# Kernel optimization log

Hardware: AMD Instinct MI355X
Metric: run time of the kernel (lower is better)

The kernel has to match this reference:

```python
import jax, jax.numpy as jnp
import numpy as np

B, T, C, H, E, L = 4, 1024, 768, 12, 4, 2
DH = C // H


def setup_inputs() -> dict:
    key = jax.random.key(0)
    ks = jax.random.split(key, 10)
    s = 0.02  # init scale; keeps unscaled-attention logits sane (source has no 1/sqrt(d))
    w = lambda k, shape: (jax.random.normal(k, shape, jnp.float32) * s)
    z = lambda shape: jnp.zeros(shape, jnp.float32)
    return dict(
        x=jax.random.normal(ks[0], (B, T, C), jnp.float32),
        gate_W=w(ks[1], (C, E)), gate_b=z((E,)),
        Wq=w(ks[2], (E, L, C, C)), bq=z((E, L, C)),
        Wk=w(ks[3], (E, L, C, C)), bk=z((E, L, C)),
        Wv=w(ks[4], (E, L, C, C)), bv=z((E, L, C)),
        Wo=w(ks[5], (E, L, C, C)), bo=z((E, L, C)),
        ln_g=jnp.ones((E, L, C), jnp.float32), ln_b=z((E, L, C)),
        Wfc=w(ks[6], (E, L, C, 4 * C)), bfc=z((E, L, 4 * C)),
        Wpr=w(ks[7], (E, L, 4 * C, C)), bpr=z((E, L, C)),
    )


def _attn(x, Wq, bq, Wk, bk, Wv, bv, Wo, bo):
    # FlashAttention3 blockwise loop == exact full softmax(Q K^T) V, NO scaling, NO mask
    q = (x @ Wq + bq).reshape(B, T, H, DH)
    k = (x @ Wk + bk).reshape(B, T, H, DH)
    v = (x @ Wv + bv).reshape(B, T, H, DH)
    s = jnp.einsum('bqhd,bkhd->bhqk', q, k)
    p = jax.nn.softmax(s, axis=-1)
    o = jnp.einsum('bhqk,bkhd->bqhd', p, v).reshape(B, T, C)
    return o @ Wo + bo


def _ln(x, g, b, eps=1e-5):
    m = x.mean(-1, keepdims=True)
    v = ((x - m) ** 2).mean(-1, keepdims=True)
    return (x - m) * jax.lax.rsqrt(v + eps) * g + b


def _expert(x, Wq, bq, Wk, bk, Wv, bv, Wo, bo, ln_g, ln_b, Wfc, bfc, Wpr, bpr):
    # Sequential(attn, layernorm, mlp) x L — no residuals, dropout=0 (eval)
    for l in range(L):
        x = _attn(x, Wq[l], bq[l], Wk[l], bk[l], Wv[l], bv[l], Wo[l], bo[l])
        x = _ln(x, ln_g[l], ln_b[l])
        h = jax.nn.gelu(x @ Wfc[l] + bfc[l], approximate=True)  # tanh GELU
        x = h @ Wpr[l] + bpr[l]
    return x


def reference(x, gate_W, gate_b, Wq, bq, Wk, bk, Wv, bv, Wo, bo,
              ln_g, ln_b, Wfc, bfc, Wpr, bpr):
    gate_probs = jax.nn.softmax(x @ gate_W + gate_b, axis=-1)  # [B,T,E]
    expert_fn = jax.vmap(_expert, in_axes=(None,) + (0,) * 14)
    eo = expert_fn(x, Wq, bq, Wk, bk, Wv, bv, Wo, bo, ln_g, ln_b, Wfc, bfc, Wpr, bpr)  # [E,B,T,C]
    return jnp.einsum('bte,ebtc->btc', gate_probs, eo)
```

## Files before the change

### kernel.cpp

```cpp
#include <hip/hip_runtime.h>

#define B_ 4
#define T_ 1024
#define C_ 768
#define H_ 12
#define E_ 4
#define L_ 2
#define DH_ 64
#define M_ (B_*T_)
#define QKVS_ (3*C_)
#define LOG2E_ 1.4426950408889634f

typedef __attribute__((ext_vector_type(8))) short bf16x8;
typedef __attribute__((ext_vector_type(4))) float f32x4;

__device__ __forceinline__ unsigned short f2bf(float f) {
  unsigned int u = __float_as_uint(f);
  unsigned int r = (u + 0x7FFFu + ((u >> 16) & 1u)) >> 16;
  return (unsigned short)r;
}
__device__ __forceinline__ float bf2f(unsigned short s) {
  return __uint_as_float(((unsigned int)s) << 16);
}
__device__ __forceinline__ unsigned int cvt_pk_bf16(float lo, float hi) {
  unsigned int r;
  asm("v_cvt_pk_bf16_f32 %0, %1, %2" : "=v"(r) : "v"(lo), "v"(hi));
  return r;
}

typedef __attribute__((address_space(1))) unsigned int gu32;
typedef __attribute__((address_space(3))) unsigned int lu32;
__device__ __forceinline__ void gld_lds16(const void* g, void* l) {
  __builtin_amdgcn_global_load_lds((gu32*)g, (lu32*)l, 16, 0, 0);
}

__device__ __forceinline__ float gelu_fast(float x) {
  float u = 0.7978845608028654f * x * (1.0f + 0.044715f * x * x);
  float d = 1.0f + exp2f(-2.8853900817779268f * u);
  return x * __builtin_amdgcn_rcpf(d);
}

template <int ACT>
__global__ __launch_bounds__(512, 2) void gemm256(
    const unsigned short* __restrict__ A, const unsigned short* __restrict__ Bt,
    const float* __restrict__ bias, unsigned short* __restrict__ D,
    int M, int N, int K, long long sA, long long sB, long long sBias, long long sD,
    float bscale)
{
  __shared__ unsigned short shA[2][256*64];
  __shared__ unsigned short shB[2][256*64];
  const int tid = threadIdx.x;
  const int lane = tid & 63, wid = tid >> 6;
  const int l15 = lane & 15, lhi = lane >> 4;
  const int wm = wid >> 2, wn = wid & 3;
  const int m0 = blockIdx.y * 256, n0 = blockIdx.x * 256;
  const int g = blockIdx.z;
  const unsigned short* Ab = A + (size_t)g * sA;
  const unsigned short* Bb = Bt + (size_t)g * sB;
  const float* biasb = bias + (size_t)g * sBias;
  unsigned short* Db = D + (size_t)g * sD;

  f32x4 acc[8][4] = {};

  const int srow = tid >> 3;
  const int schk = (((tid & 7) ^ (srow & 7)) << 3);
  auto stage = [&](int buf, int k0) {
    #pragma unroll
    for (int p = 0; p < 4; ++p)
      gld_lds16(Ab + (size_t)(m0 + p*64 + srow) * K + (k0 + schk), &shA[buf][p*4096 + tid*8]);
    #pragma unroll
    for (int p = 0; p < 4; ++p)
      gld_lds16(Bb + (size_t)(n0 + p*64 + srow) * K + (k0 + schk), &shB[buf][p*4096 + tid*8]);
  };

  const int swz = l15 & 7;
  const int ca0 = (lhi ^ swz) << 3;
  const int ca1 = ((4 + lhi) ^ swz) << 3;

  auto compute = [&](int buf) {
    #pragma unroll
    for (int kh = 0; kh < 2; ++kh) {
      const int cc = kh ? ca1 : ca0;
      bf16x8 bfrag[4];
      #pragma unroll
      for (int nf = 0; nf < 4; ++nf)
        bfrag[nf] = *(const bf16x8*)&shB[buf][(wn*64 + nf*16 + l15)*64 + cc];
      #pragma unroll
      for (int mh = 0; mh < 2; ++mh) {
        bf16x8 afr[4];
        #pragma unroll
        for (int i = 0; i < 4; ++i)
          afr[i] = *(const bf16x8*)&shA[buf][(wm*128 + (mh*4 + i)*16 + l15)*64 + cc];
        __builtin_amdgcn_s_setprio(1);
        #pragma unroll
        for (int i = 0; i < 4; ++i)
          #pragma unroll
          for (int nf = 0; nf < 4; ++nf)
            acc[mh*4+i][nf] = __builtin_amdgcn_mfma_f32_16x16x32_bf16(
                afr[i], bfrag[nf], acc[mh*4+i][nf], 0, 0, 0);
        __builtin_amdgcn_s_setprio(0);
      }
    }
  };

  const int nkt = K >> 6;
  stage(0, 0);
  stage(1, 64);

  for (int kt = 0; kt < nkt - 2; ++kt) {
    asm volatile("s_waitcnt vmcnt(8)" ::: "memory");
    __builtin_amdgcn_s_barrier();
    compute(kt & 1);
    __builtin_amdgcn_s_barrier();
    stage(kt & 1, (kt + 2) << 6);
  }
  asm volatile("s_waitcnt vmcnt(8)" ::: "memory");
  __builtin_amdgcn_s_barrier();
  compute((nkt - 2) & 1);
  asm volatile("s_waitcnt vmcnt(0)" ::: "memory");
  __builtin_amdgcn_s_barrier();
  compute((nkt - 1) & 1);

  #pragma unroll
  for (int nf = 0; nf < 4; ++nf) {
    const int col = n0 + wn*64 + nf*16 + l15;
    const float bv = bscale * biasb[col];
    #pragma unroll
    for (int mf = 0; mf < 8; ++mf) {
      const int r0 = m0 + wm*128 + mf*16 + lhi*4;
      #pragma unroll
      for (int r = 0; r < 4; ++r) {
        float v = acc[mf][nf][r] + bv;
        if (ACT == 1) v = gelu_fast(v);
        Db[(size_t)(r0 + r) * N + col] = f2bf(v);
      }
    }
  }
}

__global__ __launch_bounds__(256) void flash_attn(
    const unsigned short* __restrict__ qkv, const unsigned short* __restrict__ vt,
    unsigned short* __restrict__ o)
{
  __shared__ unsigned short shK[2][64*64];
  __shared__ unsigned short shV[2][64*64];
  __shared__ unsigned short shP[4][16*64];
  const int tid = threadIdx.x;
  const int wid = tid >> 6, lane = tid & 63;
  const int l15 = lane & 15, lhi = lane >> 4;
  const int qt = blockIdx.x, h = blockIdx.y, eb = blockIdx.z;

  const unsigned short* qrow = qkv + ((size_t)eb*T_ + qt*64 + wid*16 + l15) * QKVS_ + h*DH_;
  bf16x8 aq0 = *(const bf16x8*)(qrow + lhi*8);
  bf16x8 aq1 = *(const bf16x8*)(qrow + 32 + lhi*8);

  f32x4 oacc[4] = {};
  float lpart = 0.f;

  const int krow = tid >> 3;
  const int swzsrc = (((tid & 7) ^ (krow & 7)) << 3);
  const unsigned short* kbase = qkv + (size_t)eb*T_*QKVS_ + C_ + h*DH_;
  const unsigned short* vbase = vt + ((size_t)eb*H_ + h)*DH_*T_;

  auto stage = [&](int buf, int kt) {
    #pragma unroll
    for (int p = 0; p < 2; ++p) {
      gld_lds16(kbase + (size_t)(kt*64 + krow + p*32)*QKVS_ + swzsrc,
                &shK[buf][(p*256 + wid*64)*8]);
      gld_lds16(vbase + (size_t)(krow + p*32)*T_ + kt*64 + swzsrc,
                &shV[buf][(p*256 + wid*64)*8]);
    }
  };

  stage(0, 0);
  __syncthreads();
  int cur = 0;
  const int swzr = l15 & 7;
  const int c0 = (lhi ^ swzr) << 3;
  const int c1 = ((4 + lhi) ^ swzr) << 3;
  const int pwbase = l15*64 + ((lhi & 1) << 2);
  const int pwh = lhi >> 1;

  for (int kt = 0; kt < T_/64; ++kt) {
    if (kt + 1 < T_/64) stage(cur ^ 1, kt + 1);

    f32x4 s[4];
    #pragma unroll
    for (int kb = 0; kb < 4; ++kb) {
      const int row = (kb*16 + l15)*64;
      bf16x8 bk0 = *(const bf16x8*)&shK[cur][row + c0];
      bf16x8 bk1 = *(const bf16x8*)&shK[cur][row + c1];
      f32x4 z = {};
      z = __builtin_amdgcn_mfma_f32_16x16x32_bf16(bk0, aq0, z, 0, 0, 0);
      s[kb] = __builtin_amdgcn_mfma_f32_16x16x32_bf16(bk1, aq1, z, 0, 0, 0);
    }
    unsigned int pk0[4], pk1[4];
    #pragma unroll
    for (int kb = 0; kb < 4; ++kb) {
      #pragma unroll
      for (int r = 0; r < 4; ++r) {
        float pv = exp2f(s[kb][r]);
        s[kb][r] = pv;
        lpart += pv;
      }
      pk0[kb] = cvt_pk_bf16(s[kb][0], s[kb][1]);
      pk1[kb] = cvt_pk_bf16(s[kb][2], s[kb][3]);
    }
    #pragma unroll
    for (int kb = 0; kb < 4; ++kb) {
      const int chunk = (2*kb + pwh) ^ swzr;
      uint2 w = {pk0[kb], pk1[kb]};
      *(uint2*)&shP[wid][pwbase + chunk*8] = w;
    }
    bf16x8 pa0 = *(const bf16x8*)&shP[wid][l15*64 + c0];
    bf16x8 pa1 = *(const bf16x8*)&shP[wid][l15*64 + c1];
    #pragma unroll
    for (int n = 0; n < 4; ++n) {
      const int row = (n*16 + l15)*64;
      bf16x8 bv0 = *(const bf16x8*)&shV[cur][row + c0];
      bf16x8 bv1 = *(const bf16x8*)&shV[cur][row + c1];
      oacc[n] = __builtin_amdgcn_mfma_f32_16x16x32_bf16(pa0, bv0, oacc[n], 0, 0, 0);
      oacc[n] = __builtin_amdgcn_mfma_f32_16x16x32_bf16(pa1, bv1, oacc[n], 0, 0, 0);
    }
    __syncthreads();
    cur ^= 1;
  }
  lpart += __shfl_xor(lpart, 16);
  lpart += __shfl_xor(lpart, 32);
  float li[4];
  #pragma unroll
  for (int r = 0; r < 4; ++r) li[r] = __shfl(lpart, lhi*4 + r);
  #pragma unroll
  for (int n = 0; n < 4; ++n)
    #pragma unroll
    for (int r = 0; r < 4; ++r) {
      float v = oacc[n][r] / li[r];
      o[((size_t)eb*T_ + qt*64 + wid*16 + lhi*4 + r) * C_ + h*DH_ + n*16 + l15] = f2bf(v);
    }
}

__global__ void transpose_cast(const float* __restrict__ in, unsigned short* __restrict__ out,
                               int K, int N, long long inStride, long long outStride, float scale)
{
  __shared__ float tile[32][33];
  const float* src = in + (size_t)blockIdx.z * inStride;
  unsigned short* dst = out + (size_t)blockIdx.z * outStride;
  const int tx = threadIdx.x, ty = threadIdx.y;
  const int k0 = blockIdx.y*32, n0 = blockIdx.x*32;
  #pragma unroll
  for (int j = 0; j < 32; j += 8)
    tile[ty+j][tx] = src[(size_t)(k0+ty+j)*N + n0+tx];
  __syncthreads();
  #pragma unroll
  for (int j = 0; j < 32; j += 8)
    dst[(size_t)(n0+ty+j)*K + k0+tx] = f2bf(scale * tile[tx][ty+j]);
}

__global__ __launch_bounds__(256) void build_qkv_bias(
    const float* __restrict__ bq, const float* __restrict__ bk, const float* __restrict__ bv,
    float* __restrict__ dst, int l)
{
  const int i = blockIdx.x*256 + threadIdx.x;
  const int g = i / C_, c = i - g*C_;
  const size_t src = ((size_t)g*L_ + l)*C_ + c;
  dst[(size_t)g*QKVS_ + c]        = LOG2E_ * bq[src];
  dst[(size_t)g*QKVS_ + C_ + c]   = bk[src];
  dst[(size_t)g*QKVS_ + 2*C_ + c] = bv[src];
}

__global__ void transpose_v_kernel(const unsigned short* __restrict__ qkv, unsigned short* __restrict__ vt)
{
  __shared__ unsigned short tile[32][33];
  const int t0 = blockIdx.x * 32, d0 = blockIdx.y * 32;
  const int z = blockIdx.z;
  const int h = z % H_, eb = z / H_;
  const int tx = threadIdx.x, ty = threadIdx.y;
  #pragma unroll
  for (int j = 0; j < 32; j += 8)
    tile[ty+j][tx] = qkv[((size_t)eb*T_ + t0+ty+j)*QKVS_ + 2*C_ + h*DH_ + d0 + tx];
  __syncthreads();
  #pragma unroll
  for (int j = 0; j < 32; j += 8)
    vt[((size_t)z*DH_ + d0+ty+j)*T_ + t0 + tx] = tile[tx][ty+j];
}

__global__ __launch_bounds__(256) void ln_kernel(
    const unsigned short* __restrict__ in, unsigned short* __restrict__ out,
    const float* __restrict__ g, const float* __restrict__ b)
{
  const int row = blockIdx.x * 4 + (threadIdx.x >> 6);
  const int lane = threadIdx.x & 63;
  const int e = row >> 12;
  const unsigned short* ir = in + (size_t)row * C_;
  unsigned short* orow = out + (size_t)row * C_;
  const float* gg = g + (size_t)e * (L_*C_);
  const float* bb = b + (size_t)e * (L_*C_);
  float v[12]; float s = 0.f, s2 = 0.f;
  #pragma unroll
  for (int j = 0; j < 12; ++j) {
    float x = bf2f(ir[lane + 64*j]);
    v[j] = x; s += x; s2 += x*x;
  }
  #pragma unroll
  for (int d = 32; d; d >>= 1) { s += __shfl_xor(s, d); s2 += __shfl_xor(s2, d); }
  float mean = s * (1.f/C_);
  float var = s2 * (1.f/C_) - mean*mean;
  float rstd = rsqrtf(var + 1e-5f);
  #pragma unroll
  for (int j = 0; j < 12; ++j) {
    int c = lane + 64*j;
    orow[c] = f2bf((v[j]-mean)*rstd*gg[c] + bb[c]);
  }
}

__global__ __launch_bounds__(256) void gate_kernel(
    const float* __restrict__ x, const float* __restrict__ gw, const float* __restrict__ gb,
    float* __restrict__ gp)
{
  const int row = blockIdx.x * 4 + (threadIdx.x >> 6);
  const int lane = threadIdx.x & 63;
  const float* xr = x + (size_t)row * C_;
  float a0=0.f, a1=0.f, a2=0.f, a3=0.f;
  for (int i = lane; i < C_; i += 64) {
    float xv = xr[i];
    float4 w = ((const float4*)gw)[i];
    a0 += xv*w.x; a1 += xv*w.y; a2 += xv*w.z; a3 += xv*w.w;
  }
  #pragma unroll
  for (int d = 32; d; d >>= 1) {
    a0 += __shfl_xor(a0,d); a1 += __shfl_xor(a1,d);
    a2 += __shfl_xor(a2,d); a3 += __shfl_xor(a3,d);
  }
  if (lane == 0) {
    a0 += gb[0]; a1 += gb[1]; a2 += gb[2]; a3 += gb[3];
    float m = fmaxf(fmaxf(a0,a1), fmaxf(a2,a3));
    float e0 = __expf(a0-m), e1 = __expf(a1-m), e2 = __expf(a2-m), e3 = __expf(a3-m);
    float inv = 1.f/(e0+e1+e2+e3);
    float4 r = {e0*inv, e1*inv, e2*inv, e3*inv};
    ((float4*)gp)[row] = r;
  }
}

__global__ __launch_bounds__(256) void cast_x_kernel(const float* __restrict__ x,
                                                     unsigned short* __restrict__ xbf)
{
  const size_t i = (size_t)blockIdx.x * 256 + threadIdx.x;
  float4 v = ((const float4*)x)[i];
  ushort4 u;
  u.x = f2bf(v.x); u.y = f2bf(v.y); u.z = f2bf(v.z); u.w = f2bf(v.w);
  #pragma unroll
  for (int e = 0; e < E_; ++e)
    ((ushort4*)(xbf + (size_t)e * ((size_t)M_*C_)))[i] = u;
}

__global__ __launch_bounds__(256) void combine_kernel(
    const unsigned short* __restrict__ xbf, const float* __restrict__ gp, float* __restrict__ out)
{
  const size_t i = (size_t)blockIdx.x * 256 + threadIdx.x;
  const int row = (int)((i*4) / C_);
  float4 gpv = ((const float4*)gp)[row];
  const float* gpf = (const float*)&gpv;
  float r0=0.f, r1=0.f, r2=0.f, r3=0.f;
  #pragma unroll
  for (int e = 0; e < E_; ++e) {
    ushort4 u = ((const ushort4*)(xbf + (size_t)e*((size_t)M_*C_)))[i];
    float ge = gpf[e];
    r0 += ge*bf2f(u.x); r1 += ge*bf2f(u.y); r2 += ge*bf2f(u.z); r3 += ge*bf2f(u.w);
  }
  float4 res = {r0, r1, r2, r3};
  ((float4*)out)[i] = res;
}

extern "C" void kernel_launch(void* const* d_in, const int* in_sizes, int n_in,
                              void* d_out, int out_size, void* d_ws, size_t ws_size,
                              hipStream_t stream) {
  const float* x      = (const float*)d_in[0];
  const float* gate_W = (const float*)d_in[1];
  const float* gate_b = (const float*)d_in[2];
  const float* Wq = (const float*)d_in[3];
  const float* bq = (const float*)d_in[4];
  const float* Wk = (const float*)d_in[5];
  const float* bk = (const float*)d_in[6];
  const float* Wv = (const float*)d_in[7];
  const float* bv = (const float*)d_in[8];
  const float* Wo = (const float*)d_in[9];
  const float* bo = (const float*)d_in[10];
  const float* ln_g = (const float*)d_in[11];
  const float* ln_b = (const float*)d_in[12];
  const float* Wfc = (const float*)d_in[13];
  const float* bfc = (const float*)d_in[14];
  const float* Wpr = (const float*)d_in[15];
  const float* bpr = (const float*)d_in[16];
  float* out = (float*)d_out;

  const size_t CC  = (size_t)C_*C_;
  const size_t C4C = (size_t)C_*4*C_;
  const size_t MC  = (size_t)M_*C_;
  const size_t M4C = (size_t)M_*4*C_;

  char* p = (char*)d_ws;
  auto carve = [&](size_t bytes) { char* r = p; p += (bytes + 255) & ~(size_t)255; return r; };
  unsigned short* wqkvT = (unsigned short*)carve(E_*3*CC*2);
  unsigned short* woT   = (unsigned short*)carve(E_*CC*2);
  unsigned short* wfcT  = (unsigned short*)carve(E_*C4C*2);
  unsigned short* wprT  = (unsigned short*)carve(E_*C4C*2);
  unsigned short* xbf   = (unsigned short*)carve(E_*MC*2);
  unsigned short* r1    = (unsigned short*)carve((size_t)4*E_*MC*2);
  float* gp   = (float*)carve((size_t)M_*E_*4);
  float* bqkv = (float*)carve((size_t)E_*QKVS_*4);

  unsigned short* qkvb = r1;
  unsigned short* vtb  = r1 + (size_t)3*E_*MC;
  unsigned short* ob   = xbf;
  unsigned short* tb   = vtb;
  unsigned short* hb   = r1;

  dim3 blk256(256);
  dim3 blk512(512);
  dim3 blkT(32, 8);

  cast_x_kernel<<<dim3((unsigned)(MC/4/256)), blk256, 0, stream>>>(x, xbf);
  gate_kernel<<<dim3(M_/4), blk256, 0, stream>>>(x, gate_W, gate_b, gp);

  for (int l = 0; l < L_; ++l) {
    transpose_cast<<<dim3(24,24,E_), blkT, 0, stream>>>(Wq + l*CC, wqkvT,          C_, C_, (long long)(L_*CC), (long long)(3*CC), LOG2E_);
    transpose_cast<<<dim3(24,24,E_), blkT, 0, stream>>>(Wk + l*CC, wqkvT + CC,     C_, C_, (long long)(L_*CC), (long long)(3*CC), 1.0f);
    transpose_cast<<<dim3(24,24,E_), blkT, 0, stream>>>(Wv + l*CC, wqkvT + 2*CC,   C_, C_, (long long)(L_*CC), (long long)(3*CC), 1.0f);
    transpose_cast<<<dim3(24,24,E_), blkT, 0, stream>>>(Wo + l*CC,  woT,  C_,   C_,   (long long)(L_*CC),  (long long)CC, 1.0f);
    transpose_cast<<<dim3(96,24,E_), blkT, 0, stream>>>(Wfc + l*C4C, wfcT, C_,   4*C_, (long long)(L_*C4C), (long long)C4C, 1.0f);
    transpose_cast<<<dim3(24,96,E_), blkT, 0, stream>>>(Wpr + l*C4C, wprT, 4*C_, C_,   (long long)(L_*C4C), (long long)C4C, 1.0f);
    build_qkv_bias<<<dim3(E_*C_/256), blk256, 0, stream>>>(bq, bk, bv, bqkv, l);

    gemm256<0><<<dim3(QKVS_/256, M_/256, E_), blk512, 0, stream>>>(
        xbf, wqkvT, bqkv, qkvb, M_, QKVS_, C_, (long long)MC, (long long)(3*CC), (long long)QKVS_, (long long)M_*QKVS_, 1.0f);

    transpose_v_kernel<<<dim3(T_/32, DH_/32, E_*B_*H_), blkT, 0, stream>>>(qkvb, vtb);
    flash_attn<<<dim3(T_/64, H_, E_*B_), blk256, 0, stream>>>(qkvb, vtb, ob);

    gemm256<0><<<dim3(C_/256, M_/256, E_), blk512, 0, stream>>>(
        ob, woT, bo + l*C_, tb, M_, C_, C_, (long long)MC, (long long)CC, (long long)(L_*C_), (long long)MC, 1.0f);

    ln_kernel<<<dim3(E_*M_/4), blk256, 0, stream>>>(tb, xbf, ln_g + l*C_, ln_b + l*C_);

    gemm256<1><<<dim3(4*C_/256, M_/256, E_), blk512, 0, stream>>>(
        xbf, wfcT, bfc + l*4*C_, hb, M_, 4*C_, C_, (long long)MC, (long long)C4C, (long long)(L_*4*C_), (long long)M4C, 1.0f);
    gemm256<0><<<dim3(C_/256, M_/256, E_), blk512, 0, stream>>>(
        hb, wprT, bpr + l*C_, xbf, M_, C_, 4*C_, (long long)M4C, (long long)C4C, (long long)(L_*C_), (long long)MC, 1.0f);
  }

  combine_kernel<<<dim3((unsigned)(MC/4/256)), blk256, 0, stream>>>(xbf, gp, out);
}
```

Baseline: 1.035 ms.

## Split GEMM k-tiles into half stages with interleaved ping-pong pipeline and XCD remap

Restructures the 256x256 bf16 GEMM main loop so that each 64-wide k-tile is staged as two 32-wide halves. Global-to-LDS loads of upcoming halves are issued between the LDS fragment reads and the MFMA bursts, with barriers splitting each half into two MFMA groups. This is meant to keep loads in flight more continuously and overlap LDS reads with MFMA work. It also changes the LDS layout and swizzle to match the new fragment addressing. Finally, it remaps workgroup IDs round-robin across groups of eight, presumably for XCD/L2 locality, at the cost of many more barriers per k-tile.

```diff
diff --git a/kernel.cpp b/kernel.cpp
--- a/kernel.cpp
+++ b/kernel.cpp
@@ -47,14 +47,22 @@
     int M, int N, int K, long long sA, long long sB, long long sBias, long long sD,
     float bscale)
 {
-  __shared__ unsigned short shA[2][256*64];
-  __shared__ unsigned short shB[2][256*64];
+  __shared__ unsigned short shA[2][2][256*32];
+  __shared__ unsigned short shB[2][2][256*32];
   const int tid = threadIdx.x;
   const int lane = tid & 63, wid = tid >> 6;
   const int l15 = lane & 15, lhi = lane >> 4;
   const int wm = wid >> 2, wn = wid & 3;
-  const int m0 = blockIdx.y * 256, n0 = blockIdx.x * 256;
-  const int g = blockIdx.z;
+
+  const int gx = gridDim.x, gxy = gx * gridDim.y;
+  const int nwg = gxy * gridDim.z;
+  int flat = blockIdx.z*gxy + blockIdx.y*gx + blockIdx.x;
+  flat = (flat & 7) * (nwg >> 3) + (flat >> 3);
+  const int g = flat / gxy;
+  const int rem = flat - g*gxy;
+  const int by = rem / gx, bx = rem - by*gx;
+  const int m0 = by * 256, n0 = bx * 256;
+
   const unsigned short* Ab = A + (size_t)g * sA;
   const unsigned short* Bb = Bt + (size_t)g * sB;
   const float* biasb = bias + (size_t)g * sBias;
@@ -62,64 +70,117 @@
 
   f32x4 acc[8][4] = {};
 
-  const int srow = tid >> 3;
-  const int schk = (((tid & 7) ^ (srow & 7)) << 3);
-  auto stage = [&](int buf, int k0) {
-    #pragma unroll
-    for (int p = 0; p < 4; ++p)
-      gld_lds16(Ab + (size_t)(m0 + p*64 + srow) * K + (k0 + schk), &shA[buf][p*4096 + tid*8]);
-    #pragma unroll
-    for (int p = 0; p < 4; ++p)
-      gld_lds16(Bb + (size_t)(n0 + p*64 + srow) * K + (k0 + schk), &shB[buf][p*4096 + tid*8]);
+  const int l15h = l15 >> 1;
+  const int s8 = (((((l15 & 1) << 2) | lhi) ^ (l15h & 7)) << 3);
+  const int aoff = (wm*64 + l15h)*64 + s8;
+  const int boff = (wn*32 + l15h)*64 + s8;
+
+  const int c0 = wid*128 + lane;
+  auto stageHalf = [&](int buf, int kh, int k0k) {
+    #pragma unroll
+    for (int iss = 0; iss < 2; ++iss) {
+      const int c = c0 + iss*64;
+      const int q = c >> 3, pp = (c & 7) ^ (q & 7);
+      const int srow = (q << 1) | (pp >> 2);
+      const int skk = k0k + ((pp & 3) << 3);
+      gld_lds16(Ab + (size_t)(m0 + srow)*K + skk, &shA[buf][kh][c*8]);
+      gld_lds16(Bb + (size_t)(n0 + srow)*K + skk, &shB[buf][kh][c*8]);
+    }
   };
 
-  const int swz = l15 & 7;
-  const int ca0 = (lhi ^ swz) << 3;
-  const int ca1 = ((4 + lhi) ^ swz) << 3;
-
-  auto compute = [&](int buf) {
-    #pragma unroll
-    for (int kh = 0; kh < 2; ++kh) {
-      const int cc = kh ? ca1 : ca0;
-      bf16x8 bfrag[4];
+  bf16x8 bfrag[4], afr[4];
+  auto loadB = [&](int buf, int kh) {
+    #pragma unroll
+    for (int nf = 0; nf < 4; ++nf)
+      bfrag[nf] = *(const bf16x8*)&shB[buf][kh][boff + nf*512];
+  };
+  auto loadA = [&](int buf, int kh, int mh) {
+    #pragma unroll
+    for (int i = 0; i < 4; ++i)
+      afr[i] = *(const bf16x8*)&shA[buf][kh][aoff + (mh*4 + i)*512];
+  };
+  auto mfma16 = [&](int mh) {
+    __builtin_amdgcn_s_setprio(1);
+    #pragma unroll
+    for (int i = 0; i < 4; ++i)
       #pragma unroll
       for (int nf = 0; nf < 4; ++nf)
-        bfrag[nf] = *(const bf16x8*)&shB[buf][(wn*64 + nf*16 + l15)*64 + cc];
-      #pragma unroll
-      for (int mh = 0; mh < 2; ++mh) {
-        bf16x8 afr[4];
-        #pragma unroll
-        for (int i = 0; i < 4; ++i)
-          afr[i] = *(const bf16x8*)&shA[buf][(wm*128 + (mh*4 + i)*16 + l15)*64 + cc];
-        __builtin_amdgcn_s_setprio(1);
-        #pragma unroll
-        for (int i = 0; i < 4; ++i)
-          #pragma unroll
-          for (int nf = 0; nf < 4; ++nf)
-            acc[mh*4+i][nf] = __builtin_amdgcn_mfma_f32_16x16x32_bf16(
-                afr[i], bfrag[nf], acc[mh*4+i][nf], 0, 0, 0);
-        __builtin_amdgcn_s_setprio(0);
-      }
-    }
+        acc[mh*4+i][nf] = __builtin_amdgcn_mfma_f32_16x16x32_bf16(
+            afr[i], bfrag[nf], acc[mh*4+i][nf], 0, 0, 0);
+    __builtin_amdgcn_s_setprio(0);
   };
 
   const int nkt = K >> 6;
-  stage(0, 0);
-  stage(1, 64);
-
-  for (int kt = 0; kt < nkt - 2; ++kt) {
-    asm volatile("s_waitcnt vmcnt(8)" ::: "memory");
-    __builtin_amdgcn_s_barrier();
-    compute(kt & 1);
-    __builtin_amdgcn_s_barrier();
-    stage(kt & 1, (kt + 2) << 6);
-  }
+
+  stageHalf(0, 0, 0);
+  stageHalf(0, 1, 32);
+  stageHalf(1, 0, 64);
   asm volatile("s_waitcnt vmcnt(8)" ::: "memory");
   __builtin_amdgcn_s_barrier();
-  compute((nkt - 2) & 1);
-  asm volatile("s_waitcnt vmcnt(0)" ::: "memory");
-  __builtin_amdgcn_s_barrier();
-  compute((nkt - 1) & 1);
+
+  for (int kt = 0; kt <= nkt - 3; ++kt) {
+    const int buf = kt & 1;
+    loadB(buf, 0); loadA(buf, 0, 0);
+    stageHalf(buf ^ 1, 1, ((kt + 1) << 6) + 32);
+    __builtin_amdgcn_s_barrier();
+    mfma16(0);
+    __builtin_amdgcn_s_barrier();
+    loadA(buf, 0, 1);
+    __builtin_amdgcn_s_barrier();
+    mfma16(1);
+    asm volatile("s_waitcnt vmcnt(8)" ::: "memory");
+    __builtin_amdgcn_s_barrier();
+    loadB(buf, 1); loadA(buf, 1, 0);
+    stageHalf(buf, 0, (kt + 2) << 6);
+    __builtin_amdgcn_s_barrier();
+    mfma16(0);
+    __builtin_amdgcn_s_barrier();
+    loadA(buf, 1, 1);
+    __builtin_amdgcn_s_barrier();
+    mfma16(1);
+    asm volatile("s_waitcnt vmcnt(8)" ::: "memory");
+    __builtin_amdgcn_s_barrier();
+  }
+  {
+    const int buf = (nkt - 2) & 1;
+    loadB(buf, 0); loadA(buf, 0, 0);
+    stageHalf(buf ^ 1, 1, ((nkt - 1) << 6) + 32);
+    __builtin_amdgcn_s_barrier();
+    mfma16(0);
+    __builtin_amdgcn_s_barrier();
+    loadA(buf, 0, 1);
+    __builtin_amdgcn_s_barrier();
+    mfma16(1);
+    asm volatile("s_waitcnt vmcnt(8)" ::: "memory");
+    __builtin_amdgcn_s_barrier();
+    loadB(buf, 1); loadA(buf, 1, 0);
+    __builtin_amdgcn_s_barrier();
+    mfma16(0);
+    __builtin_amdgcn_s_barrier();
+    loadA(buf, 1, 1);
+    __builtin_amdgcn_s_barrier();
+    mfma16(1);
+    asm volatile("s_waitcnt vmcnt(4)" ::: "memory");
+    __builtin_amdgcn_s_barrier();
+  }
+  {
+    const int buf = (nkt - 1) & 1;
+    loadB(buf, 0); loadA(buf, 0, 0);
+    __builtin_amdgcn_s_barrier();
+    mfma16(0);
+    __builtin_amdgcn_s_barrier();
+    loadA(buf, 0, 1);
+    __builtin_amdgcn_s_barrier();
+    mfma16(1);
+    asm volatile("s_waitcnt vmcnt(0)" ::: "memory");
+    __builtin_amdgcn_s_barrier();
+    loadB(buf, 1); loadA(buf, 1, 0);
+    __builtin_amdgcn_s_barrier();
+    mfma16(0);
+    __builtin_amdgcn_s_barrier();
+    loadA(buf, 1, 1);
+    mfma16(1);
+  }
 
   #pragma unroll
   for (int nf = 0; nf < 4; ++nf) {
```

Result: no change. 1.044 ms (+0.9%).

## Restructure GEMM into 4-slot half-K pipeline with interleaved staging and XCD-aware block remap

Applied to the files above, without the earlier changes.

Splits each 64-wide K tile into two 32-wide halves held in a 4-slot LDS ring, and interleaves global-to-LDS loads for future halves inside each compute phase, each phase fenced by barriers. It also remaps the flat workgroup index so consecutive tiles are spread across the 8 chiplets, and changes the LDS swizzle to match the new row-pair layout. The aim is finer-grained overlap of loads with MFMA work and better L2 locality. The cost is more barriers per K step and a more intricate vmcnt schedule that could stall if it is mis-tuned.

```diff
diff --git a/kernel.cpp b/kernel.cpp
--- a/kernel.cpp
+++ b/kernel.cpp
@@ -47,14 +47,22 @@
     int M, int N, int K, long long sA, long long sB, long long sBias, long long sD,
     float bscale)
 {
-  __shared__ unsigned short shA[2][256*64];
-  __shared__ unsigned short shB[2][256*64];
+  __shared__ unsigned short shA[4][256*32];
+  __shared__ unsigned short shB[4][256*32];
   const int tid = threadIdx.x;
   const int lane = tid & 63, wid = tid >> 6;
   const int l15 = lane & 15, lhi = lane >> 4;
   const int wm = wid >> 2, wn = wid & 3;
-  const int m0 = blockIdx.y * 256, n0 = blockIdx.x * 256;
-  const int g = blockIdx.z;
+
+  const int gx = gridDim.x, gxy = gx * gridDim.y;
+  const int nwg = gxy * gridDim.z;
+  int flat = blockIdx.z*gxy + blockIdx.y*gx + blockIdx.x;
+  flat = (flat & 7) * (nwg >> 3) + (flat >> 3);
+  const int g = flat / gxy;
+  const int rem = flat - g*gxy;
+  const int by = rem / gx, bx = rem - by*gx;
+  const int m0 = by * 256, n0 = bx * 256;
+
   const unsigned short* Ab = A + (size_t)g * sA;
   const unsigned short* Bb = Bt + (size_t)g * sB;
   const float* biasb = bias + (size_t)g * sBias;
@@ -62,64 +70,74 @@
 
   f32x4 acc[8][4] = {};
 
-  const int srow = tid >> 3;
-  const int schk = (((tid & 7) ^ (srow & 7)) << 3);
-  auto stage = [&](int buf, int k0) {
-    #pragma unroll
-    for (int p = 0; p < 4; ++p)
-      gld_lds16(Ab + (size_t)(m0 + p*64 + srow) * K + (k0 + schk), &shA[buf][p*4096 + tid*8]);
-    #pragma unroll
-    for (int p = 0; p < 4; ++p)
-      gld_lds16(Bb + (size_t)(n0 + p*64 + srow) * K + (k0 + schk), &shB[buf][p*4096 + tid*8]);
+  const int l15h = l15 >> 1;
+  const int s8 = (((((l15 & 1) << 2) | lhi) ^ (l15h & 7)) << 3);
+  const int arp = wm*64;
+  const int brp = wn*32;
+
+  auto stageA = [&](int slot, int kh) {
+    const int kb = kh << 5;
+    #pragma unroll
+    for (int iss = 0; iss < 2; ++iss) {
+      const int c = tid + iss*512;
+      const int q = c >> 3, pp = (c & 7) ^ (q & 7);
+      gld_lds16(Ab + (size_t)(m0 + (q << 1) + (pp >> 2))*K + kb + ((pp & 3) << 3),
+                &shA[slot][c*8]);
+    }
   };
-
-  const int swz = l15 & 7;
-  const int ca0 = (lhi ^ swz) << 3;
-  const int ca1 = ((4 + lhi) ^ swz) << 3;
-
-  auto compute = [&](int buf) {
-    #pragma unroll
-    for (int kh = 0; kh < 2; ++kh) {
-      const int cc = kh ? ca1 : ca0;
-      bf16x8 bfrag[4];
+  auto stageB = [&](int slot, int kh) {
+    const int kb = kh << 5;
+    #pragma unroll
+    for (int iss = 0; iss < 2; ++iss) {
+      const int c = tid + iss*512;
+      const int q = c >> 3, pp = (c & 7) ^ (q & 7);
+      gld_lds16(Bb + (size_t)(n0 + (q << 1) + (pp >> 2))*K + kb + ((pp & 3) << 3),
+                &shB[slot][c*8]);
+    }
+  };
+
+  auto phase = [&](int slot, int mh, int stSel, int stSlot, int stKh, int vmN) {
+    bf16x8 afr[4], bfr[4];
+    #pragma unroll
+    for (int i = 0; i < 4; ++i)
+      afr[i] = *(const bf16x8*)&shA[slot][(arp + mh*32 + i*8 + l15h)*64 + s8];
+    #pragma unroll
+    for (int nf = 0; nf < 4; ++nf)
+      bfr[nf] = *(const bf16x8*)&shB[slot][(brp + nf*8 + l15h)*64 + s8];
+    if (stSel == 1) stageA(stSlot, stKh);
+    else if (stSel == 2) stageB(stSlot, stKh);
+    if (vmN == 4) asm volatile("s_waitcnt vmcnt(4)" ::: "memory");
+    else if (vmN == 0) asm volatile("s_waitcnt vmcnt(0)" ::: "memory");
+    __builtin_amdgcn_s_barrier();
+    __builtin_amdgcn_s_setprio(1);
+    #pragma unroll
+    for (int i = 0; i < 4; ++i)
       #pragma unroll
       for (int nf = 0; nf < 4; ++nf)
-        bfrag[nf] = *(const bf16x8*)&shB[buf][(wn*64 + nf*16 + l15)*64 + cc];
-      #pragma unroll
-      for (int mh = 0; mh < 2; ++mh) {
-        bf16x8 afr[4];
-        #pragma unroll
-        for (int i = 0; i < 4; ++i)
-          afr[i] = *(const bf16x8*)&shA[buf][(wm*128 + (mh*4 + i)*16 + l15)*64 + cc];
-        __builtin_amdgcn_s_setprio(1);
-        #pragma unroll
-        for (int i = 0; i < 4; ++i)
-          #pragma unroll
-          for (int nf = 0; nf < 4; ++nf)
-            acc[mh*4+i][nf] = __builtin_amdgcn_mfma_f32_16x16x32_bf16(
-                afr[i], bfrag[nf], acc[mh*4+i][nf], 0, 0, 0);
-        __builtin_amdgcn_s_setprio(0);
-      }
-    }
+        acc[mh*4+i][nf] = __builtin_amdgcn_mfma_f32_16x16x32_bf16(
+            afr[i], bfr[nf], acc[mh*4+i][nf], 0, 0, 0);
+    __builtin_amdgcn_s_setprio(0);
+    __builtin_amdgcn_s_barrier();
   };
 
   const int nkt = K >> 6;
-  stage(0, 0);
-  stage(1, 64);
-
-  for (int kt = 0; kt < nkt - 2; ++kt) {
-    asm volatile("s_waitcnt vmcnt(8)" ::: "memory");
-    __builtin_amdgcn_s_barrier();
-    compute(kt & 1);
-    __builtin_amdgcn_s_barrier();
-    stage(kt & 1, (kt + 2) << 6);
-  }
-  asm volatile("s_waitcnt vmcnt(8)" ::: "memory");
+  const int nkh = nkt << 1;
+
+  stageA(0, 0); stageB(0, 0);
+  stageA(1, 1); stageB(1, 1);
+  stageA(2, 2); stageB(2, 2);
+  asm volatile("s_waitcnt vmcnt(4)" ::: "memory");
   __builtin_amdgcn_s_barrier();
-  compute((nkt - 2) & 1);
-  asm volatile("s_waitcnt vmcnt(0)" ::: "memory");
-  __builtin_amdgcn_s_barrier();
-  compute((nkt - 1) & 1);
+
+  for (int k = 0; k < nkt; ++k) {
+    const int s0 = (2*k) & 3, s1 = s0 + 1;
+    const int m3 = 2*k + 3, m4 = 2*k + 4;
+    const bool f3 = m3 < nkh, f4 = m4 < nkh;
+    phase(s0, 0, f3 ? 1 : 0, m3 & 3, m3, -1);
+    phase(s0, 1, f3 ? 2 : 0, m3 & 3, m3, -1);
+    phase(s1, 0, f4 ? 1 : 0, m4 & 3, m4, -1);
+    phase(s1, 1, f4 ? 2 : 0, m4 & 3, m4, f4 ? 4 : (f3 ? 0 : -1));
+  }
 
   #pragma unroll
   for (int nf = 0; nf < 4; ++nf) {
```

New measurement: 1.003 ms. 1.03x faster.
